# Optimization experiments

Hardware: AMD Instinct MI355X
Metric: run time of the kernel (lower is better)

The kernel has to match this reference:

```python
import jax, jax.numpy as jnp
import numpy as np

TEMPERATURE = 0.07
EPS = 1e-12


def setup_inputs() -> dict:
    key = jax.random.key(0)
    k1, k2 = jax.random.split(key)
    N, D = 8192, 1024
    features = jax.random.normal(k1, (N, D), dtype=jnp.float32)
    labels = jax.random.randint(k2, (N,), 0, 1000, dtype=jnp.int64)
    return {"features": features, "labels": labels}


def reference(features, labels):
    # L2-normalize rows (matches F.normalize(dim=1) with its eps clamp)
    norm = jnp.maximum(jnp.linalg.norm(features, axis=1, keepdims=True), 1e-12)
    f = features / norm
    n = f.shape[0]
    # [N, N] similarity
    sim = jnp.matmul(f, f.T) / TEMPERATURE
    # positive-pair mask from labels
    mask = (labels[:, None] == labels[None, :]).astype(sim.dtype)
    # denominator excludes self-similarity via (1 - eye)
    not_self = 1.0 - jnp.eye(n, dtype=sim.dtype)
    exp_sim = jnp.exp(sim) * not_self
    log_prob = sim - jnp.log(exp_sim.sum(axis=1, keepdims=True) + EPS)
    loss = -(mask * log_prob).sum(axis=1) / (mask.sum(axis=1) + EPS)
    return loss.mean()
```

## Files before the change

### kernel.cpp

```cpp
#include <hip/hip_runtime.h>
#include <hip/hip_bf16.h>

#define N_ROWS 8192
#define DIM 1024
#define TEMP_INV (1.0f / 0.07f)

typedef __attribute__((ext_vector_type(4))) int i32x4;

__device__ inline void gload_lds16(const void* g, void* l) {
    __builtin_amdgcn_global_load_lds(
        (const __attribute__((address_space(1))) void*)g,
        (__attribute__((address_space(3))) void*)l,
        16, 0, 0);
}

__global__ __launch_bounds__(256) void knorm(const float* __restrict__ X,
                                             char* __restrict__ Q,
                                             float* __restrict__ SC,
                                             float* __restrict__ S1,
                                             float* __restrict__ S2,
                                             float* __restrict__ CNT) {
    const int row = blockIdx.x;
    const int t = threadIdx.x;
    const float* x = X + (size_t)row * DIM;
    float4 v = reinterpret_cast<const float4*>(x)[t];
    float ss = v.x * v.x + v.y * v.y + v.z * v.z + v.w * v.w;
    float mx = fmaxf(fmaxf(fabsf(v.x), fabsf(v.y)), fmaxf(fabsf(v.z), fabsf(v.w)));
    #pragma unroll
    for (int off = 32; off > 0; off >>= 1) {
        ss += __shfl_down(ss, off);
        mx = fmaxf(mx, __shfl_down(mx, off));
    }
    __shared__ float redS[4], redM[4];
    if ((t & 63) == 0) { redS[t >> 6] = ss; redM[t >> 6] = mx; }
    __syncthreads();
    float tot = redS[0] + redS[1] + redS[2] + redS[3];
    float amax = fmaxf(fmaxf(redM[0], redM[1]), fmaxf(redM[2], redM[3]));
    amax = fmaxf(amax, 1e-20f);
    const float norm = fmaxf(sqrtf(tot), 1e-12f);
    const float qmul = 127.0f / amax;
    const float scale = amax / (127.0f * norm);
    int q0 = (int)rintf(v.x * qmul);
    int q1 = (int)rintf(v.y * qmul);
    int q2 = (int)rintf(v.z * qmul);
    int q3 = (int)rintf(v.w * qmul);
    q0 = min(max(q0, -127), 127); q1 = min(max(q1, -127), 127);
    q2 = min(max(q2, -127), 127); q3 = min(max(q3, -127), 127);
    const unsigned packed = (unsigned)(q0 & 0xff) | ((unsigned)(q1 & 0xff) << 8) |
                            ((unsigned)(q2 & 0xff) << 16) | ((unsigned)(q3 & 0xff) << 24);
    reinterpret_cast<unsigned*>(Q + (size_t)row * DIM)[t] = packed;
    if (t == 0) SC[row] = scale;
    if (t == 1) { S1[row] = 0.f; S2[row] = 0.f; CNT[row] = 0.f; }
}

__global__ __launch_bounds__(256) void kgemm(const char* __restrict__ Q,
                                             const float* __restrict__ SC,
                                             const int* __restrict__ labels,
                                             float* __restrict__ S1,
                                             float* __restrict__ S2,
                                             float* __restrict__ CNT) {
    constexpr int BM = 128, BK = 128;
    __shared__ __align__(16) char As[BM * BK];
    __shared__ __align__(16) char Bs[BM * BK];
    __shared__ int labR[BM];
    __shared__ int labC[BM];
    __shared__ float scR[BM];
    __shared__ float scCs[BM];

    const int bid0 = blockIdx.x;
    const int bid = (bid0 & 7) * 260 + (bid0 >> 3);
    int a = (int)((sqrtf(8.0f * (float)bid + 1.0f) - 1.0f) * 0.5f);
    while ((a + 1) * (a + 2) / 2 <= bid) ++a;
    while (a * (a + 1) / 2 > bid) --a;
    const int bx = a;
    const int by = bid - a * (a + 1) / 2;
    const bool diag = (bx == by);
    const int rowBase = by * BM;
    const int colBase = bx * BM;

    const int t = threadIdx.x;
    const int lane = t & 63;
    const int wid = t >> 6;
    const int wr = wid >> 1;
    const int wc = wid & 1;
    const int l16 = lane & 15;
    const int g16 = lane >> 4;

    if (t < 128) { labR[t] = labels[rowBase + t]; scR[t] = SC[rowBase + t]; }
    else { labC[t - 128] = labels[colBase + (t - 128)]; scCs[t - 128] = SC[colBase + (t - 128)]; }

    i32x4 acc[4][4];
    #pragma unroll
    for (int m = 0; m < 4; ++m)
        #pragma unroll
        for (int n = 0; n < 4; ++n)
            acc[m][n] = i32x4{0, 0, 0, 0};

    const int srow = t >> 3;
    const int scolL = (t & 7) * 16;
    const int xorb = (l16 & 7) << 4;

    for (int kt = 0; kt < DIM / BK; ++kt) {
        const int k0 = kt * BK;
        #pragma unroll
        for (int i = 0; i < 4; ++i) {
            const int r = i * 32 + srow;
            const int sg = scolL ^ ((r & 7) << 4);
            gload_lds16(Q + (size_t)(rowBase + r) * DIM + k0 + sg, &As[r * BK + scolL]);
            gload_lds16(Q + (size_t)(colBase + r) * DIM + k0 + sg, &Bs[r * BK + scolL]);
        }
        __syncthreads();

        #pragma unroll
        for (int kk = 0; kk < 2; ++kk) {
            const int ck = (kk * 64 + g16 * 16) ^ xorb;
            i32x4 av[4], bv[4];
            #pragma unroll
            for (int m = 0; m < 4; ++m)
                av[m] = *reinterpret_cast<const i32x4*>(&As[(wr * 64 + m * 16 + l16) * BK + ck]);
            #pragma unroll
            for (int n = 0; n < 4; ++n)
                bv[n] = *reinterpret_cast<const i32x4*>(&Bs[(wc * 64 + n * 16 + l16) * BK + ck]);
            #pragma unroll
            for (int m = 0; m < 4; ++m)
                #pragma unroll
                for (int n = 0; n < 4; ++n)
                    acc[m][n] = __builtin_amdgcn_mfma_i32_16x16x64_i8(av[m], bv[n], acc[m][n], 0, 0, 0);
        }
        __syncthreads();
    }

    int labCn[4];
    float scCn[4];
    #pragma unroll
    for (int n = 0; n < 4; ++n) {
        const int c = wc * 64 + n * 16 + l16;
        labCn[n] = labC[c];
        scCn[n] = scCs[c] * TEMP_INV;
    }

    const unsigned long long grpmask = 0xFFFFull << (g16 * 16);

    float colE[4]  = {0.f, 0.f, 0.f, 0.f};
    float colS2[4] = {0.f, 0.f, 0.f, 0.f};
    float colC[4]  = {0.f, 0.f, 0.f, 0.f};

    #pragma unroll
    for (int m = 0; m < 4; ++m) {
        const int rloc = wr * 64 + m * 16 + g16 * 4;
        #pragma unroll
        for (int reg = 0; reg < 4; ++reg) {
            const int row = rowBase + rloc + reg;
            const int labRow = labR[rloc + reg];
            const float sRow = scR[rloc + reg];
            float e = 0.f, s2 = 0.f, c = 0.f;
            #pragma unroll
            for (int n = 0; n < 4; ++n) {
                const float sim = (float)acc[m][n][reg] * sRow * scCn[n];
                const int col = colBase + wc * 64 + n * 16 + l16;
                const float ex = __expf(sim);
                const bool same = (labRow == labCn[n]);
                if (diag) {
                    if (row != col) e += ex;
                } else {
                    e += ex;
                    colE[n] += ex;
                }
                if (same) {
                    s2 += sim; c += 1.0f;
                    if (!diag) { colS2[n] += sim; colC[n] += 1.0f; }
                }
            }
            const unsigned long long bal = __ballot(c != 0.f);
            const bool doS = (bal & grpmask) != 0ull;
            #pragma unroll
            for (int off = 1; off < 16; off <<= 1) e += __shfl_xor(e, off);
            if (doS) {
                #pragma unroll
                for (int off = 1; off < 16; off <<= 1) {
                    s2 += __shfl_xor(s2, off);
                    c  += __shfl_xor(c, off);
                }
            }
            if (l16 == 0) {
                atomicAdd(&S1[row], e);
                if (doS) {
                    atomicAdd(&S2[row], s2);
                    atomicAdd(&CNT[row], c);
                }
            }
        }
    }

    if (!diag) {
        #pragma unroll
        for (int n = 0; n < 4; ++n) {
            float ce = colE[n], cs = colS2[n], cc = colC[n];
            const unsigned long long bal = __ballot(cc != 0.f);
            #pragma unroll
            for (int off = 16; off < 64; off <<= 1) ce += __shfl_xor(ce, off);
            if (bal) {
                #pragma unroll
                for (int off = 16; off < 64; off <<= 1) {
                    cs += __shfl_xor(cs, off);
                    cc += __shfl_xor(cc, off);
                }
            }
            if (g16 == 0) {
                const int col = colBase + wc * 64 + n * 16 + l16;
                atomicAdd(&S1[col], ce);
                if (bal) {
                    atomicAdd(&S2[col], cs);
                    atomicAdd(&CNT[col], cc);
                }
            }
        }
    }
}

__global__ __launch_bounds__(1024) void kfinal(const float* __restrict__ S1,
                                               const float* __restrict__ S2,
                                               const float* __restrict__ CNT,
                                               float* __restrict__ out) {
    const int t = threadIdx.x;
    float a = 0.f;
    for (int i = t; i < N_ROWS; i += 1024) {
        const float cnt = CNT[i];
        const float ld = logf(S1[i] + 1e-12f);
        a += (cnt * ld - S2[i]) / (cnt + 1e-12f);
    }
    #pragma unroll
    for (int off = 32; off > 0; off >>= 1) a += __shfl_down(a, off);
    __shared__ float red[16];
    if ((t & 63) == 0) red[t >> 6] = a;
    __syncthreads();
    if (t == 0) {
        float s = 0.f;
        #pragma unroll
        for (int i = 0; i < 16; ++i) s += red[i];
        out[0] = s / (float)N_ROWS;
    }
}

extern "C" void kernel_launch(void* const* d_in, const int* in_sizes, int n_in,
                              void* d_out, int out_size, void* d_ws, size_t ws_size,
                              hipStream_t stream) {
    const float* feat = (const float*)d_in[0];
    const int* labels = (const int*)d_in[1];
    float* out = (float*)d_out;

    char* Q = (char*)d_ws;
    float* SC = (float*)((char*)d_ws + (size_t)N_ROWS * DIM);
    float* S1 = SC + N_ROWS;
    float* S2 = S1 + N_ROWS;
    float* CNT = S2 + N_ROWS;

    constexpr int NT = N_ROWS / 128;
    constexpr int NBLK = NT * (NT + 1) / 2;

    knorm<<<N_ROWS, 256, 0, stream>>>(feat, Q, SC, S1, S2, CNT);
    kgemm<<<NBLK, 256, 0, stream>>>(Q, SC, labels, S1, S2, CNT);
    kfinal<<<1, 1024, 0, stream>>>(S1, S2, CNT, out);
}
```

Before: 77.98 us.

## Load int8 GEMM operands directly from global into registers, drop LDS staging

Removes the LDS tiles and global_load_lds staging in the int8 similarity GEMM. Each wave now reads its A/B fragments straight from global memory into registers in a fully unrolled K loop, which eliminates the per-tile barriers. Launch bounds now request 4 blocks per SM for higher occupancy. The cost is that operand data is no longer shared across waves through LDS, so every wave issues redundant global/L2 loads and the register footprint of the unrolled loop grows.

```diff
diff --git a/kernel.cpp b/kernel.cpp
--- a/kernel.cpp
+++ b/kernel.cpp
@@ -6,13 +6,6 @@
 #define TEMP_INV (1.0f / 0.07f)
 
 typedef __attribute__((ext_vector_type(4))) int i32x4;
-
-__device__ inline void gload_lds16(const void* g, void* l) {
-    __builtin_amdgcn_global_load_lds(
-        (const __attribute__((address_space(1))) void*)g,
-        (__attribute__((address_space(3))) void*)l,
-        16, 0, 0);
-}
 
 __global__ __launch_bounds__(256) void knorm(const float* __restrict__ X,
                                              char* __restrict__ Q,
@@ -53,15 +46,13 @@
     if (t == 1) { S1[row] = 0.f; S2[row] = 0.f; CNT[row] = 0.f; }
 }
 
-__global__ __launch_bounds__(256) void kgemm(const char* __restrict__ Q,
-                                             const float* __restrict__ SC,
-                                             const int* __restrict__ labels,
-                                             float* __restrict__ S1,
-                                             float* __restrict__ S2,
-                                             float* __restrict__ CNT) {
-    constexpr int BM = 128, BK = 128;
-    __shared__ __align__(16) char As[BM * BK];
-    __shared__ __align__(16) char Bs[BM * BK];
+__global__ __launch_bounds__(256, 4) void kgemm(const char* __restrict__ Q,
+                                                const float* __restrict__ SC,
+                                                const int* __restrict__ labels,
+                                                float* __restrict__ S1,
+                                                float* __restrict__ S2,
+                                                float* __restrict__ CNT) {
+    constexpr int BM = 128;
     __shared__ int labR[BM];
     __shared__ int labC[BM];
     __shared__ float scR[BM];
@@ -88,6 +79,16 @@
 
     if (t < 128) { labR[t] = labels[rowBase + t]; scR[t] = SC[rowBase + t]; }
     else { labC[t - 128] = labels[colBase + (t - 128)]; scCs[t - 128] = SC[colBase + (t - 128)]; }
+    __syncthreads();
+
+    const char* aRow[4];
+    const char* bRow[4];
+    #pragma unroll
+    for (int m = 0; m < 4; ++m)
+        aRow[m] = Q + (size_t)(rowBase + wr * 64 + m * 16 + l16) * DIM + g16 * 16;
+    #pragma unroll
+    for (int n = 0; n < 4; ++n)
+        bRow[n] = Q + (size_t)(colBase + wc * 64 + n * 16 + l16) * DIM + g16 * 16;
 
     i32x4 acc[4][4];
     #pragma unroll
@@ -96,38 +97,24 @@
         for (int n = 0; n < 4; ++n)
             acc[m][n] = i32x4{0, 0, 0, 0};
 
-    const int srow = t >> 3;
-    const int scolL = (t & 7) * 16;
-    const int xorb = (l16 & 7) << 4;
-
-    for (int kt = 0; kt < DIM / BK; ++kt) {
-        const int k0 = kt * BK;
-        #pragma unroll
-        for (int i = 0; i < 4; ++i) {
-            const int r = i * 32 + srow;
-            const int sg = scolL ^ ((r & 7) << 4);
-            gload_lds16(Q + (size_t)(rowBase + r) * DIM + k0 + sg, &As[r * BK + scolL]);
-            gload_lds16(Q + (size_t)(colBase + r) * DIM + k0 + sg, &Bs[r * BK + scolL]);
-        }
-        __syncthreads();
-
+    #pragma unroll
+    for (int kt = 0; kt < 8; ++kt) {
         #pragma unroll
         for (int kk = 0; kk < 2; ++kk) {
-            const int ck = (kk * 64 + g16 * 16) ^ xorb;
+            const int ko = kt * 128 + kk * 64;
             i32x4 av[4], bv[4];
             #pragma unroll
             for (int m = 0; m < 4; ++m)
-                av[m] = *reinterpret_cast<const i32x4*>(&As[(wr * 64 + m * 16 + l16) * BK + ck]);
+                av[m] = *reinterpret_cast<const i32x4*>(aRow[m] + ko);
             #pragma unroll
             for (int n = 0; n < 4; ++n)
-                bv[n] = *reinterpret_cast<const i32x4*>(&Bs[(wc * 64 + n * 16 + l16) * BK + ck]);
+                bv[n] = *reinterpret_cast<const i32x4*>(bRow[n] + ko);
             #pragma unroll
             for (int m = 0; m < 4; ++m)
                 #pragma unroll
                 for (int n = 0; n < 4; ++n)
                     acc[m][n] = __builtin_amdgcn_mfma_i32_16x16x64_i8(av[m], bv[n], acc[m][n], 0, 0, 0);
         }
-        __syncthreads();
     }
 
     int labCn[4];
```

Result: slower. 171.9 us (+120.5%).
